# Optimization experiments

Measured on AMD Instinct MI355X. Metric: run time of the kernel, lower is better.

The kernel has to match this reference:

```python
import jax, jax.numpy as jnp
import numpy as np

D = 128; H = 8; DH = D // H
N = 50000; B = 8; MAXN = N // B
E = 400000
NG_G = 4; NG_L = 4; NG = NG_G + NG_L
DFF = 2 * D


def _ln(x, eps=1e-5):
    m = x.mean(-1, keepdims=True)
    v = ((x - m) ** 2).mean(-1, keepdims=True)
    return (x - m) * jax.lax.rsqrt(v + eps)


def _mha(q, k, v, in_w, in_b, out_w, out_b):
    # torch nn.MultiheadAttention (batch_first, eval) with packed in_proj
    Bq, Lq, d = q.shape; Lk = k.shape[1]
    wq, wk, wv = jnp.split(in_w, 3, axis=0)
    bq, bk, bv = jnp.split(in_b, 3)
    Q = (q @ wq.T + bq).reshape(Bq, Lq, H, DH).transpose(0, 2, 1, 3)
    K = (k @ wk.T + bk).reshape(Bq, Lk, H, DH).transpose(0, 2, 1, 3)
    V = (v @ wv.T + bv).reshape(Bq, Lk, H, DH).transpose(0, 2, 1, 3)
    A = jax.nn.softmax(jnp.einsum('bhqd,bhkd->bhqk', Q, K) / np.float32(np.sqrt(DH)), axis=-1)
    O = jnp.einsum('bhqk,bhkd->bhqd', A, V).transpose(0, 2, 1, 3).reshape(Bq, Lq, d)
    return O @ out_w.T + out_b, A.mean(axis=1)  # averaged attn weights over heads


def _tconv(x, src, dst, Wq, bq, Wk, bk, Wv, bv, Wskip, bskip, Wbeta):
    # PyG TransformerConv(d, d//H, heads=H, beta=True): edge-wise gather-attend-scatter
    n = x.shape[0]
    q = (x @ Wq.T + bq)[dst].reshape(-1, H, DH)   # [E,H,DH] query at target node
    k = (x @ Wk.T + bk)[src].reshape(-1, H, DH)
    v = (x @ Wv.T + bv)[src].reshape(-1, H, DH)
    logits = (q * k).sum(-1) / np.float32(np.sqrt(DH))  # [E,H]
    m = jax.ops.segment_max(logits, dst, num_segments=n)
    m = jnp.where(jnp.isfinite(m), m, 0.0)
    a = jnp.exp(logits - m[dst])
    s = jax.ops.segment_sum(a, dst, num_segments=n)
    alpha = a / (s[dst] + 1e-16)                  # per-target-node softmax (PyG softmax)
    out = jax.ops.segment_sum(v * alpha[..., None], dst, num_segments=n).reshape(n, D)
    xr = x @ Wskip.T + bskip                      # root weight
    beta = jax.nn.sigmoid(jnp.concatenate([out, xr, out - xr], axis=-1) @ Wbeta.T)
    return beta * xr + (1.0 - beta) * out


def setup_inputs() -> dict:
    key = jax.random.key(0)
    ks = jax.random.split(key, 16)
    w = lambda i, shape, s=0.05: jax.random.normal(ks[i], shape, jnp.float32) * s
    return dict(
        x=w(0, (N, D), 1.0),
        edge_index=jax.random.randint(ks[1], (2, E), 0, N),
        global_h=w(2, (B, NG, D), 1.0),
        batch=jnp.repeat(jnp.arange(B, dtype=jnp.int32), MAXN),  # sorted, even split
        n_global_tokens_global=NG_G,
        n_global_tokens_local=NG_L,
        Wq=w(3, (D, D)), bq=jnp.zeros((D,), jnp.float32),
        Wk=w(4, (D, D)), bk=jnp.zeros((D,), jnp.float32),
        Wv=w(5, (D, D)), bv=jnp.zeros((D,), jnp.float32),
        Wskip=w(6, (D, D)), bskip=jnp.zeros((D,), jnp.float32),
        Wbeta=w(7, (1, 3 * D)),
        ng_in_w=w(8, (3 * D, D)), ng_in_b=jnp.zeros((3 * D,), jnp.float32),
        ng_out_w=w(9, (D, D)), ng_out_b=jnp.zeros((D,), jnp.float32),
        gn_in_w=w(10, (3 * D, D)), gn_in_b=jnp.zeros((3 * D,), jnp.float32),
        gn_out_w=w(11, (D, D)), gn_out_b=jnp.zeros((D,), jnp.float32),
        W1=w(12, (DFF, D)), b1=jnp.zeros((DFF,), jnp.float32),
        W2=w(13, (D, DFF)), b2=jnp.zeros((D,), jnp.float32),
    )


def reference(x, edge_index, global_h, batch, n_global_tokens_global, n_global_tokens_local,
              Wq, bq, Wk, bk, Wv, bv, Wskip, bskip, Wbeta,
              ng_in_w, ng_in_b, ng_out_w, ng_out_b,
              gn_in_w, gn_in_b, gn_out_w, gn_out_b,
              W1, b1, W2, b2):
    src, dst = edge_index[0], edge_index[1]
    h_local = _tconv(x, src, dst, Wq, bq, Wk, bk, Wv, bv, Wskip, bskip, Wbeta)
    x = _ln(x + h_local)
    Bg = global_h.shape[0]
    # to_dense_batch: batch is sorted with equal-size graphs -> mask all True, pure reshape
    dense_x = x.reshape(Bg, -1, D)
    global_out, attn_w = _mha(global_h, dense_x, dense_x, ng_in_w, ng_in_b, ng_out_w, ng_out_b)
    global_h = _ln(global_h + global_out)
    nodes_out, _ = _mha(dense_x, global_h, global_h, gn_in_w, gn_in_b, gn_out_w, gn_out_b)
    dense_x = _ln(dense_x + nodes_out)
    x = dense_x.reshape(-1, D)  # un-scatter (even split -> reshape)
    ff = jax.nn.relu(x @ W1.T + b1) @ W2.T + b2
    x = _ln(x + ff)
    # attention regularization, vectorized over the per-graph python loop
    ls = n_global_tokens_global
    le = ls + n_global_tokens_local
    P = attn_w[:, ls:le, :]                      # [B, K, max_n], all nodes valid
    Pn = P / (P.sum(-1, keepdims=True) + 1e-8)
    G = jnp.einsum('bkn,bmn->bkm', Pn, Pn)       # [B, K, K]
    Kt = le - ls
    off = (G.sum(axis=(1, 2)) - jnp.einsum('bkk->b', G)) / (Kt * Kt - Kt)
    reg = off.mean()
    return x, global_h, reg
```

## Files before the change

kernel.cpp:

```cpp
#include <hip/hip_runtime.h>
#include <math.h>

#define D 128
#define H 8
#define NGT 8
#define LSTOK 4
#define NCH 4

typedef short bf16x8 __attribute__((ext_vector_type(8)));
typedef float f32x4  __attribute__((ext_vector_type(4)));

__device__ __forceinline__ short f2bf(float f) {
  union { float f; unsigned u; } v; v.f = f;
  unsigned r = v.u + 0x7FFFu + ((v.u >> 16) & 1u);
  return (short)(r >> 16);
}
__device__ __forceinline__ float bf2f(short s) {
  union { unsigned u; float f; } v;
  v.u = ((unsigned)(unsigned short)s) << 16;
  return v.f;
}
__device__ __forceinline__ float4 bf4(bf16x8 v, int lo) {
  return make_float4(bf2f(v[lo]), bf2f(v[lo + 1]), bf2f(v[lo + 2]), bf2f(v[lo + 3]));
}
__device__ __forceinline__ unsigned pk2(float a, float b) {
  return ((unsigned)(unsigned short)f2bf(b) << 16) | (unsigned short)f2bf(a);
}

__device__ __forceinline__ float dot4(float4 a, float4 b) {
  return a.x*b.x + a.y*b.y + a.z*b.z + a.w*b.w;
}
__device__ __forceinline__ float4 scale_madd(float4 a, float sc, float4 v, float p) {
  return make_float4(fmaf(p, v.x, a.x*sc), fmaf(p, v.y, a.y*sc),
                     fmaf(p, v.z, a.z*sc), fmaf(p, v.w, a.w*sc));
}
__device__ __forceinline__ float4 comb4(float4 a, float e1, float4 c, float e2) {
  return make_float4(a.x*e1 + c.x*e2, a.y*e1 + c.y*e2, a.z*e1 + c.z*e2, a.w*e1 + c.w*e2);
}
__device__ __forceinline__ float4 shfl_xor4(float4 v, int off) {
  return make_float4(__shfl_xor(v.x, off), __shfl_xor(v.y, off),
                     __shfl_xor(v.z, off), __shfl_xor(v.w, off));
}

struct CvtArgs {
  const float* s[10];
  short*       d[10];
  int          n[10];
};

__global__ void cvt_weights(CvtArgs a) {
  int which = blockIdx.y;
  const float* s = a.s[which];
  short* d = a.d[which];
  int n = a.n[which];
  int i = (blockIdx.x * 256 + threadIdx.x) * 4;
  if (i + 3 < n) {
    float4 v = *(const float4*)(s + i);
    d[i]     = f2bf(v.x);
    d[i + 1] = f2bf(v.y);
    d[i + 2] = f2bf(v.z);
    d[i + 3] = f2bf(v.w);
  }
}

__global__ void cvt_x(const float* __restrict__ s, short* __restrict__ d, int n) {
  int i = (blockIdx.x * 256 + threadIdx.x) * 8;
  if (i + 7 < n) {
    float4 a = *(const float4*)(s + i);
    float4 b = *(const float4*)(s + i + 4);
    bf16x8 v;
    v[0] = f2bf(a.x); v[1] = f2bf(a.y); v[2] = f2bf(a.z); v[3] = f2bf(a.w);
    v[4] = f2bf(b.x); v[5] = f2bf(b.y); v[6] = f2bf(b.z); v[7] = f2bf(b.w);
    *(bf16x8*)(d + i) = v;
  }
}

__global__ void concat_bias4(const float* __restrict__ b0, const float* __restrict__ b1,
                             const float* __restrict__ b2, const float* __restrict__ b3,
                             float* __restrict__ out) {
  int t = threadIdx.x;
  out[t] = b0[t]; out[128 + t] = b1[t]; out[256 + t] = b2[t]; out[384 + t] = b3[t];
}

#define EPST 72
template<int K>
__global__ void __launch_bounds__(256) gemm_direct(const short* __restrict__ A,
    const short* __restrict__ Wb, const float* __restrict__ bias,
    short* __restrict__ out16, int C16, int s16,
    float* __restrict__ out32, int s32,
    int Nrows, int Ccols, int relu)
{
  __shared__ short eplds[4][64 * EPST];
  const int t = threadIdx.x;
  const int wid = t >> 6, lane = t & 63;
  const int rowBase = blockIdx.x * 128 + (wid >> 1) * 64;
  const int colBase = blockIdx.y * 128 + (wid & 1) * 64;
  const int lrow = lane & 15;
  const int lk = (lane >> 4) * 8;

  f32x4 acc[4][4];
  f32x4 z4 = {0.f, 0.f, 0.f, 0.f};
#pragma unroll
  for (int m = 0; m < 4; m++)
#pragma unroll
    for (int n = 0; n < 4; n++) acc[m][n] = z4;

  const short* ap[4];
#pragma unroll
  for (int m = 0; m < 4; ++m) {
    int ar = rowBase + m * 16 + lrow;
    if (ar >= Nrows) ar = Nrows - 1;
    ap[m] = A + (size_t)ar * K + lk;
  }
  const short* wp[4];
#pragma unroll
  for (int n = 0; n < 4; ++n)
    wp[n] = Wb + (size_t)(colBase + n * 16 + lrow) * K + lk;

#pragma unroll
  for (int kb = 0; kb < K; kb += 32) {
    bf16x8 af[4], bfr[4];
#pragma unroll
    for (int m = 0; m < 4; ++m) af[m] = *(const bf16x8*)(ap[m] + kb);
#pragma unroll
    for (int n = 0; n < 4; ++n) bfr[n] = *(const bf16x8*)(wp[n] + kb);
#pragma unroll
    for (int m = 0; m < 4; ++m)
#pragma unroll
      for (int n = 0; n < 4; ++n)
        acc[m][n] = __builtin_amdgcn_mfma_f32_16x16x32_bf16(af[m], bfr[n], acc[m][n], 0, 0, 0);
  }

  const int ccol = lane & 15;
  const int rquad = (lane >> 4) * 4;
  if (colBase < C16) {
    short* lds = eplds[wid];
#pragma unroll
    for (int n = 0; n < 4; ++n) {
      float bb = bias[colBase + n * 16 + ccol];
      int col = n * 16 + ccol;
#pragma unroll
      for (int m = 0; m < 4; ++m) {
        int r0 = m * 16 + rquad;
#pragma unroll
        for (int r = 0; r < 4; ++r) {
          float v = acc[m][n][r] + bb;
          if (relu) v = fmaxf(v, 0.f);
          lds[(r0 + r) * EPST + col] = f2bf(v);
        }
      }
    }
    const int jr = lane >> 3, jc = lane & 7;
#pragma unroll
    for (int i = 0; i < 8; ++i) {
      int row = i * 8 + jr;
      int gr = rowBase + row;
      if (gr < Nrows) {
        bf16x8 v = *(const bf16x8*)(lds + row * EPST + jc * 8);
        *(bf16x8*)(out16 + (size_t)gr * s16 + colBase + jc * 8) = v;
      }
    }
  } else {
#pragma unroll
    for (int n = 0; n < 4; ++n) {
      int col = colBase + n * 16 + ccol;
      float bb = bias[col];
#pragma unroll
      for (int m = 0; m < 4; ++m) {
        int row0 = rowBase + m * 16 + rquad;
#pragma unroll
        for (int r = 0; r < 4; ++r) {
          int gr = row0 + r;
          if (gr < Nrows) {
            float v = acc[m][n][r] + bb;
            if (relu) v = fmaxf(v, 0.f);
            out32[(size_t)gr * s32 + (col - C16)] = v;
          }
        }
      }
    }
  }
}

#define FFST 264
__global__ void __launch_bounds__(256) gemm_ff(const short* __restrict__ A,
    const short* __restrict__ W1b, const float* __restrict__ b1,
    const short* __restrict__ W2b, const float* __restrict__ b2,
    float* __restrict__ out, int Nrows)
{
  __shared__ short flds[128 * FFST];
  const int t = threadIdx.x;
  const int wid = t >> 6, lane = t & 63;
  const int rowL = (wid >> 1) * 64;
  const int rowBase = blockIdx.x * 128 + rowL;
  const int lrow = lane & 15;
  const int lk = (lane >> 4) * 8;
  const int ccol = lane & 15;
  const int rquad = (lane >> 4) * 4;
  f32x4 z4 = {0.f, 0.f, 0.f, 0.f};

  const short* ap[4];
#pragma unroll
  for (int m = 0; m < 4; ++m) {
    int ar = rowBase + m * 16 + lrow;
    if (ar >= Nrows) ar = Nrows - 1;
    ap[m] = A + (size_t)ar * 128 + lk;
  }

  for (int cb = 0; cb < 2; ++cb) {
    int colBase = cb * 128 + (wid & 1) * 64;
    f32x4 acc[4][4];
#pragma unroll
    for (int m = 0; m < 4; m++)
#pragma unroll
      for (int n = 0; n < 4; n++) acc[m][n] = z4;
    const short* wp[4];
#pragma unroll
    for (int n = 0; n < 4; ++n)
      wp[n] = W1b + (size_t)(colBase + n * 16 + lrow) * 128 + lk;
#pragma unroll
    for (int kb = 0; kb < 128; kb += 32) {
      bf16x8 af[4], bfr[4];
#pragma unroll
      for (int m = 0; m < 4; ++m) af[m] = *(const bf16x8*)(ap[m] + kb);
#pragma unroll
      for (int n = 0; n < 4; ++n) bfr[n] = *(const bf16x8*)(wp[n] + kb);
#pragma unroll
      for (int m = 0; m < 4; ++m)
#pragma unroll
        for (int n = 0; n < 4; ++n)
          acc[m][n] = __builtin_amdgcn_mfma_f32_16x16x32_bf16(af[m], bfr[n], acc[m][n], 0, 0, 0);
    }
#pragma unroll
    for (int n = 0; n < 4; ++n) {
      int col = colBase + n * 16 + ccol;
      float bb = b1[col];
#pragma unroll
      for (int m = 0; m < 4; ++m) {
        int r0 = rowL + m * 16 + rquad;
#pragma unroll
        for (int r = 0; r < 4; ++r) {
          float v = fmaxf(acc[m][n][r] + bb, 0.f);
          flds[(r0 + r) * FFST + col] = f2bf(v);
        }
      }
    }
  }
  __syncthreads();

  {
    int colBase = (wid & 1) * 64;
    f32x4 acc[4][4];
#pragma unroll
    for (int m = 0; m < 4; m++)
#pragma unroll
      for (int n = 0; n < 4; n++) acc[m][n] = z4;
    const short* wp[4];
#pragma unroll
    for (int n = 0; n < 4; ++n)
      wp[n] = W2b + (size_t)(colBase + n * 16 + lrow) * 256 + lk;
#pragma unroll
    for (int kb = 0; kb < 256; kb += 32) {
      bf16x8 af[4], bfr[4];
#pragma unroll
      for (int m = 0; m < 4; ++m)
        af[m] = *(const bf16x8*)(flds + (rowL + m * 16 + lrow) * FFST + kb + lk);
#pragma unroll
      for (int n = 0; n < 4; ++n) bfr[n] = *(const bf16x8*)(wp[n] + kb);
#pragma unroll
      for (int m = 0; m < 4; ++m)
#pragma unroll
        for (int n = 0; n < 4; ++n)
          acc[m][n] = __builtin_amdgcn_mfma_f32_16x16x32_bf16(af[m], bfr[n], acc[m][n], 0, 0, 0);
    }
#pragma unroll
    for (int n = 0; n < 4; ++n) {
      int col = colBase + n * 16 + ccol;
      float bb = b2[col];
#pragma unroll
      for (int m = 0; m < 4; ++m) {
        int row0 = rowBase + m * 16 + rquad;
#pragma unroll
        for (int r = 0; r < 4; ++r) {
          int gr = row0 + r;
          if (gr < Nrows) out[(size_t)gr * 128 + col] = acc[m][n][r] + bb;
        }
      }
    }
  }
}

#define QST 136
__global__ void __launch_bounds__(256) gemm_node(const short* __restrict__ A,
    const short* __restrict__ GnQb, const float* __restrict__ gnbq,
    const float* __restrict__ Kg, const float* __restrict__ Vg,
    const short* __restrict__ GnOb, const float* __restrict__ gnbo,
    float* __restrict__ out, int Nrows, int MAXN)
{
  __shared__ short qlds[128 * QST];
  __shared__ float kg[2][NGT * 128];
  __shared__ float vg[2][NGT * 128];
  const int t = threadIdx.x;
  const int wid = t >> 6, lane = t & 63;
  const int rowL = (wid >> 1) * 64;
  const int n0 = blockIdx.x * 128;
  const int rowBase = n0 + rowL;
  const int colBase = (wid & 1) * 64;
  const int lrow = lane & 15;
  const int lk = (lane >> 4) * 8;
  const int ccol = lane & 15;
  const int rquad = (lane >> 4) * 4;
  f32x4 z4 = {0.f, 0.f, 0.f, 0.f};

  int b0 = n0 / MAXN;
  int nlast = n0 + 127; if (nlast >= Nrows) nlast = Nrows - 1;
  int bLast = nlast / MAXN;
  int nb = (bLast != b0) ? 2 : 1;
  for (int bi = 0; bi < nb; ++bi) {
    size_t gb = (size_t)((b0 + bi) * NGT) * 128;
    int i = t * 4;
    *(float4*)&kg[bi][i] = *(const float4*)(Kg + gb + i);
    *(float4*)&vg[bi][i] = *(const float4*)(Vg + gb + i);
  }

  {
    f32x4 acc[4][4];
#pragma unroll
    for (int m = 0; m < 4; m++)
#pragma unroll
      for (int n = 0; n < 4; n++) acc[m][n] = z4;
    const short* ap[4];
#pragma unroll
    for (int m = 0; m < 4; ++m) {
      int ar = rowBase + m * 16 + lrow;
      if (ar >= Nrows) ar = Nrows - 1;
      ap[m] = A + (size_t)ar * 128 + lk;
    }
    const short* wp[4];
#pragma unroll
    for (int n = 0; n < 4; ++n)
      wp[n] = GnQb + (size_t)(colBase + n * 16 + lrow) * 128 + lk;
#pragma unroll
    for (int kb = 0; kb < 128; kb += 32) {
      bf16x8 af[4], bfr[4];
#pragma unroll
      for (int m = 0; m < 4; ++m) af[m] = *(const bf16x8*)(ap[m] + kb);
#pragma unroll
      for (int n = 0; n < 4; ++n) bfr[n] = *(const bf16x8*)(wp[n] + kb);
#pragma unroll
      for (int m = 0; m < 4; ++m)
#pragma unroll
        for (int n = 0; n < 4; ++n)
          acc[m][n] = __builtin_amdgcn_mfma_f32_16x16x32_bf16(af[m], bfr[n], acc[m][n], 0, 0, 0);
    }
#pragma unroll
    for (int n = 0; n < 4; ++n) {
      int col = colBase + n * 16 + ccol;
      float bb = gnbq[col];
#pragma unroll
      for (int m = 0; m < 4; ++m) {
        int r0 = rowL + m * 16 + rquad;
#pragma unroll
        for (int r = 0; r < 4; ++r)
          qlds[(r0 + r) * QST + col] = f2bf(acc[m][n][r] + bb);
      }
    }
  }
  __syncthreads();

#pragma unroll
  for (int u = 0; u < 4; ++u) {
    int unit = t + u * 256;
    int row = unit >> 3, h = unit & 7;
    int grow = n0 + row;
    if (grow < Nrows) {
      int bi = (grow / MAXN) - b0;
      short* qp = qlds + row * QST + h * 16;
      bf16x8 qa = *(const bf16x8*)(qp);
      bf16x8 qb = *(const bf16x8*)(qp + 8);
      float4 q0 = bf4(qa, 0), q1 = bf4(qa, 4), q2 = bf4(qb, 0), q3 = bf4(qb, 4);
      float l[NGT];
      float mx = -3.0e38f;
#pragma unroll
      for (int tk = 0; tk < NGT; tk++) {
        const float4* k4 = (const float4*)(&kg[bi][tk * 128 + h * 16]);
        float d = dot4(q0, k4[0]) + dot4(q1, k4[1]) + dot4(q2, k4[2]) + dot4(q3, k4[3]);
        l[tk] = d * 0.25f;
        mx = fmaxf(mx, l[tk]);
      }
      float s = 0.f;
#pragma unroll
      for (int tk = 0; tk < NGT; tk++) { l[tk] = expf(l[tk] - mx); s += l[tk]; }
      float inv = 1.f / s;
      float4 a0 = make_float4(0, 0, 0, 0), a1 = a0, a2 = a0, a3 = a0;
#pragma unroll
      for (int tk = 0; tk < NGT; tk++) {
        float p = l[tk] * inv;
        const float4* v4 = (const float4*)(&vg[bi][tk * 128 + h * 16]);
        a0 = scale_madd(a0, 1.f, v4[0], p);
        a1 = scale_madd(a1, 1.f, v4[1], p);
        a2 = scale_madd(a2, 1.f, v4[2], p);
        a3 = scale_madd(a3, 1.f, v4[3], p);
      }
      unsigned* o = (unsigned*)qp;
      o[0] = pk2(a0.x, a0.y); o[1] = pk2(a0.z, a0.w);
      o[2] = pk2(a1.x, a1.y); o[3] = pk2(a1.z, a1.w);
      o[4] = pk2(a2.x, a2.y); o[5] = pk2(a2.z, a2.w);
      o[6] = pk2(a3.x, a3.y); o[7] = pk2(a3.z, a3.w);
    }
  }
  __syncthreads();

  {
    f32x4 acc[4][4];
#pragma unroll
    for (int m = 0; m < 4; m++)
#pragma unroll
      for (int n = 0; n < 4; n++) acc[m][n] = z4;
    const short* wp[4];
#pragma unroll
    for (int n = 0; n < 4; ++n)
      wp[n] = GnOb + (size_t)(colBase + n * 16 + lrow) * 128 + lk;
#pragma unroll
    for (int kb = 0; kb < 128; kb += 32) {
      bf16x8 af[4], bfr[4];
#pragma unroll
      for (int m = 0; m < 4; ++m)
        af[m] = *(const bf16x8*)(qlds + (rowL + m * 16 + lrow) * QST + kb + lk);
#pragma unroll
      for (int n = 0; n < 4; ++n) bfr[n] = *(const bf16x8*)(wp[n] + kb);
#pragma unroll
      for (int m = 0; m < 4; ++m)
#pragma unroll
        for (int n = 0; n < 4; ++n)
          acc[m][n] = __builtin_amdgcn_mfma_f32_16x16x32_bf16(af[m], bfr[n], acc[m][n], 0, 0, 0);
    }
#pragma unroll
    for (int n = 0; n < 4; ++n) {
      int col = colBase + n * 16 + ccol;
      float bb = gnbo[col];
#pragma unroll
      for (int m = 0; m < 4; ++m) {
        int row0 = rowBase + m * 16 + rquad;
#pragma unroll
        for (int r = 0; r < 4; ++r) {
          int gr = row0 + r;
          if (gr < Nrows) out[(size_t)gr * 128 + col] = acc[m][n][r] + bb;
        }
      }
    }
  }
}

__global__ void gemm_small(const float* __restrict__ A, const float* __restrict__ W,
                           const float* __restrict__ bias, float* __restrict__ out, int M)
{
  int r = blockIdx.x;
  int c = threadIdx.x;
  __shared__ float as[128];
  as[c] = A[(size_t)r * 128 + c];
  __syncthreads();
  float acc = bias[c];
  const float* wr = W + (size_t)c * 128;
#pragma unroll 4
  for (int k = 0; k < 128; k++) acc += as[k] * wr[k];
  out[(size_t)r * 128 + c] = acc;
}

__global__ void count_deg(const int* __restrict__ dst, int* __restrict__ deg, int E) {
  int e = blockIdx.x * 256 + threadIdx.x;
  if (e < E) atomicAdd(&deg[dst[e]], 1);
}

__global__ void scan_pass1(const int* __restrict__ deg, int* __restrict__ bsum, int N) {
  int t = threadIdx.x, lane = t & 63, wid = t >> 6;
  int idx = blockIdx.x * 1024 + t * 4;
  int4 v = {0, 0, 0, 0};
  if (idx + 3 < N) v = *(const int4*)(deg + idx);
  else {
    if (idx < N) v.x = deg[idx];
    if (idx + 1 < N) v.y = deg[idx + 1];
    if (idx + 2 < N) v.z = deg[idx + 2];
    if (idx + 3 < N) v.w = deg[idx + 3];
  }
  int s = v.x + v.y + v.z + v.w;
#pragma unroll
  for (int off = 32; off >= 1; off >>= 1) s += __shfl_xor(s, off);
  __shared__ int ws[4];
  if (lane == 0) ws[wid] = s;
  __syncthreads();
  if (t == 0) bsum[blockIdx.x] = ws[0] + ws[1] + ws[2] + ws[3];
}

__global__ void scan_pass2(int* __restrict__ bsum, int SB) {
  __shared__ int sh[1024];
  int t = threadIdx.x;
  sh[t] = (t < SB) ? bsum[t] : 0;
  __syncthreads();
  for (int off = 1; off < 1024; off <<= 1) {
    int v = (t >= off) ? sh[t - off] : 0;
    __syncthreads();
    sh[t] += v;
    __syncthreads();
  }
  if (t < SB) bsum[t] = (t == 0) ? 0 : sh[t - 1];
}

__global__ void scan_pass3(const int* __restrict__ deg, const int* __restrict__ bsum,
                           int* __restrict__ row_start, int* __restrict__ cursor,
                           int N, int E)
{
  int t = threadIdx.x, lane = t & 63, wid = t >> 6;
  int idx = blockIdx.x * 1024 + t * 4;
  int4 v = {0, 0, 0, 0};
  if (idx + 3 < N) v = *(const int4*)(deg + idx);
  else {
    if (idx < N) v.x = deg[idx];
    if (idx + 1 < N) v.y = deg[idx + 1];
    if (idx + 2 < N) v.z = deg[idx + 2];
    if (idx + 3 < N) v.w = deg[idx + 3];
  }
  int ts = v.x + v.y + v.z + v.w;
  int x = ts;
#pragma unroll
  for (int off = 1; off < 64; off <<= 1) {
    int y = __shfl_up(x, off);
    if (lane >= off) x += y;
  }
  __shared__ int ws[4];
  if (lane == 63) ws[wid] = x;
  __syncthreads();
  int woff = 0;
  for (int i = 0; i < wid; i++) woff += ws[i];
  int p = bsum[blockIdx.x] + woff + (x - ts);
  if (idx < N)     { row_start[idx] = p; cursor[idx] = p; }     p += v.x;
  if (idx + 1 < N) { row_start[idx + 1] = p; cursor[idx + 1] = p; } p += v.y;
  if (idx + 2 < N) { row_start[idx + 2] = p; cursor[idx + 2] = p; } p += v.z;
  if (idx + 3 < N) { row_start[idx + 3] = p; cursor[idx + 3] = p; }
  if (blockIdx.x == 0 && t == 0) row_start[N] = E;
}

__global__ void fill_edges(const int* __restrict__ dst, const int* __restrict__ src,
                           int* __restrict__ cursor, int* __restrict__ edge_src, int E) {
  int e = blockIdx.x * 256 + threadIdx.x;
  if (e < E) {
    int p = atomicAdd(&cursor[dst[e]], 1);
    edge_src[p] = src[e];
  }
}

__global__ void tconv_attn(const short* __restrict__ qkvb,
                           const int* __restrict__ row_start,
                           const int* __restrict__ edge_src,
                           float* __restrict__ out, int N)
{
  int gid = blockIdx.x * 256 + threadIdx.x;
  if (gid >= N * H) return;
  int n = gid >> 3, h = gid & 7;
  const short* qp = qkvb + (size_t)n * 512 + h * 16;
  bf16x8 qa = *(const bf16x8*)(qp);
  bf16x8 qb = *(const bf16x8*)(qp + 8);
  float4 q0 = bf4(qa, 0), q1 = bf4(qa, 4), q2 = bf4(qb, 0), q3 = bf4(qb, 4);
  int e0 = row_start[n], e1 = row_start[n + 1];

  float mA = -3.0e38f, sA = 0.f;
  float4 A0 = make_float4(0, 0, 0, 0), A1 = A0, A2 = A0, A3 = A0;
  float mB = -3.0e38f, sB = 0.f;
  float4 B0 = A0, B1 = A0, B2 = A0, B3 = A0;

  int ei = e0;
  for (; ei + 1 < e1; ei += 2) {
    int sn0 = edge_src[ei], sn1 = edge_src[ei + 1];
    const short* kp0 = qkvb + (size_t)sn0 * 512 + 128 + h * 16;
    const short* kp1 = qkvb + (size_t)sn1 * 512 + 128 + h * 16;
    bf16x8 k00 = *(const bf16x8*)(kp0);
    bf16x8 k01 = *(const bf16x8*)(kp0 + 8);
    bf16x8 k10 = *(const bf16x8*)(kp1);
    bf16x8 k11 = *(const bf16x8*)(kp1 + 8);
    float d0 = (dot4(q0, bf4(k00, 0)) + dot4(q1, bf4(k00, 4))
              + dot4(q2, bf4(k01, 0)) + dot4(q3, bf4(k01, 4))) * 0.25f;
    float d1 = (dot4(q0, bf4(k10, 0)) + dot4(q1, bf4(k10, 4))
              + dot4(q2, bf4(k11, 0)) + dot4(q3, bf4(k11, 4))) * 0.25f;
    bf16x8 v00 = *(const bf16x8*)(kp0 + 128);
    bf16x8 v01 = *(const bf16x8*)(kp0 + 136);
    bf16x8 v10 = *(const bf16x8*)(kp1 + 128);
    bf16x8 v11 = *(const bf16x8*)(kp1 + 136);
    float mn0 = fmaxf(mA, d0);
    float sc0 = expf(mA - mn0), p0 = expf(d0 - mn0);
    A0 = scale_madd(A0, sc0, bf4(v00, 0), p0);
    A1 = scale_madd(A1, sc0, bf4(v00, 4), p0);
    A2 = scale_madd(A2, sc0, bf4(v01, 0), p0);
    A3 = scale_madd(A3, sc0, bf4(v01, 4), p0);
    sA = sA * sc0 + p0; mA = mn0;
    float mn1 = fmaxf(mB, d1);
    float sc1 = expf(mB - mn1), p1 = expf(d1 - mn1);
    B0 = scale_madd(B0, sc1, bf4(v10, 0), p1);
    B1 = scale_madd(B1, sc1, bf4(v10, 4), p1);
    B2 = scale_madd(B2, sc1, bf4(v11, 0), p1);
    B3 = scale_madd(B3, sc1, bf4(v11, 4), p1);
    sB = sB * sc1 + p1; mB = mn1;
  }
  if (ei < e1) {
    int sn0 = edge_src[ei];
    const short* kp0 = qkvb + (size_t)sn0 * 512 + 128 + h * 16;
    bf16x8 k00 = *(const bf16x8*)(kp0);
    bf16x8 k01 = *(const bf16x8*)(kp0 + 8);
    float d0 = (dot4(q0, bf4(k00, 0)) + dot4(q1, bf4(k00, 4))
              + dot4(q2, bf4(k01, 0)) + dot4(q3, bf4(k01, 4))) * 0.25f;
    bf16x8 v00 = *(const bf16x8*)(kp0 + 128);
    bf16x8 v01 = *(const bf16x8*)(kp0 + 136);
    float mn0 = fmaxf(mA, d0);
    float sc0 = expf(mA - mn0), p0 = expf(d0 - mn0);
    A0 = scale_madd(A0, sc0, bf4(v00, 0), p0);
    A1 = scale_madd(A1, sc0, bf4(v00, 4), p0);
    A2 = scale_madd(A2, sc0, bf4(v01, 0), p0);
    A3 = scale_madd(A3, sc0, bf4(v01, 4), p0);
    sA = sA * sc0 + p0; mA = mn0;
  }
  float mn = fmaxf(mA, mB);
  float eA = expf(mA - mn), eB = expf(mB - mn);
  float s = sA * eA + sB * eB;
  float4 a0 = comb4(A0, eA, B0, eB);
  float4 a1 = comb4(A1, eA, B1, eB);
  float4 a2 = comb4(A2, eA, B2, eB);
  float4 a3 = comb4(A3, eA, B3, eB);
  float inv = 1.f / (s + 1e-16f);
  float4* o4 = (float4*)(out + (size_t)n * 128 + h * 16);
  o4[0] = make_float4(a0.x * inv, a0.y * inv, a0.z * inv, a0.w * inv);
  o4[1] = make_float4(a1.x * inv, a1.y * inv, a1.z * inv, a1.w * inv);
  o4[2] = make_float4(a2.x * inv, a2.y * inv, a2.z * inv, a2.w * inv);
  o4[3] = make_float4(a3.x * inv, a3.y * inv, a3.z * inv, a3.w * inv);
}

__global__ void gate_ln(const float* __restrict__ x, const float* __restrict__ att,
                        const short* __restrict__ qkvb, const float* __restrict__ Wb,
                        float* __restrict__ x1, short* __restrict__ x1b, int N)
{
  int wid = threadIdx.x >> 6, lane = threadIdx.x & 63;
  int n = blockIdx.x * 4 + wid;
  if (n >= N) return;
  size_t base = (size_t)n * 128 + lane * 2;
  float2 o = *(const float2*)(att + base);
  unsigned ru = *(const unsigned*)(qkvb + (size_t)n * 512 + 384 + lane * 2);
  float2 r = make_float2(bf2f((short)(ru & 0xFFFF)), bf2f((short)(ru >> 16)));
  float2 xv = *(const float2*)(x + base);
  float2 w0 = *(const float2*)(Wb + lane * 2);
  float2 w1 = *(const float2*)(Wb + 128 + lane * 2);
  float2 w2 = *(const float2*)(Wb + 256 + lane * 2);
  float ts = o.x * w0.x + o.y * w0.y + r.x * w1.x + r.y * w1.y
           + (o.x - r.x) * w2.x + (o.y - r.y) * w2.y;
#pragma unroll
  for (int mm = 32; mm >= 1; mm >>= 1) ts += __shfl_xor(ts, mm);
  float beta = 1.f / (1.f + expf(-ts));
  float2 y;
  y.x = xv.x + beta * r.x + (1.f - beta) * o.x;
  y.y = xv.y + beta * r.y + (1.f - beta) * o.y;
  float sm = y.x + y.y;
#pragma unroll
  for (int mm = 32; mm >= 1; mm >>= 1) sm += __shfl_xor(sm, mm);
  float mean = sm * (1.f / 128.f);
  float dx = y.x - mean, dy = y.y - mean;
  float vs = dx * dx + dy * dy;
#pragma unroll
  for (int mm = 32; mm >= 1; mm >>= 1) vs += __shfl_xor(vs, mm);
  float rstd = rsqrtf(vs * (1.f / 128.f) + 1e-5f);
  float ox = dx * rstd, oy = dy * rstd;
  *(float2*)(x1 + base) = make_float2(ox, oy);
  *(unsigned*)(x1b + base) = pk2(ox, oy);
}

__global__ void ln_add(const float* __restrict__ a, const float* __restrict__ b,
                       float* __restrict__ out, short* __restrict__ out16, int R)
{
  int wid = threadIdx.x >> 6, lane = threadIdx.x & 63;
  int r = blockIdx.x * 4 + wid;
  if (r >= R) return;
  size_t base = (size_t)r * 128 + lane * 2;
  float2 av = *(const float2*)(a + base);
  float2 bv = *(const float2*)(b + base);
  float2 y = make_float2(av.x + bv.x, av.y + bv.y);
  float sm = y.x + y.y;
#pragma unroll
  for (int mm = 32; mm >= 1; mm >>= 1) sm += __shfl_xor(sm, mm);
  float mean = sm * (1.f / 128.f);
  float dx = y.x - mean, dy = y.y - mean;
  float vs = dx * dx + dy * dy;
#pragma unroll
  for (int mm = 32; mm >= 1; mm >>= 1) vs += __shfl_xor(vs, mm);
  float rstd = rsqrtf(vs * (1.f / 128.f) + 1e-5f);
  float ox = dx * rstd, oy = dy * rstd;
  *(float2*)(out + base) = make_float2(ox, oy);
  if (out16) *(unsigned*)(out16 + base) = pk2(ox, oy);
}

__global__ void glob_part(const float* __restrict__ Qg, const short* __restrict__ kv,
                          float* __restrict__ Plog,
                          float* __restrict__ pm, float* __restrict__ ps,
                          float* __restrict__ pacc, int MAXN)
{
  int blk = blockIdx.x;
  int ch = blockIdx.y;
  int h = blk & 7, g = (blk >> 3) & 7, b = blk >> 6;
  int lane = threadIdx.x;
  const float4* q4 = (const float4*)(Qg + (size_t)(b * NGT + g) * 128 + h * 16);
  float4 q0 = q4[0], q1 = q4[1], q2 = q4[2], q3 = q4[3];
  int chunk = (MAXN + NCH - 1) / NCH;
  int n0 = ch * chunk;
  int n1 = n0 + chunk; if (n1 > MAXN) n1 = MAXN;
  float* plrow = (g >= LSTOK) ? Plog + (((size_t)(b * 4 + g - LSTOK)) * H + h) * MAXN : nullptr;
  float m = -3.0e38f, s = 0.f;
  float4 a0 = make_float4(0, 0, 0, 0), a1 = a0, a2 = a0, a3 = a0;
  for (int n = n0 + lane; n < n1; n += 64) {
    const short* kp = kv + ((size_t)(b * MAXN + n)) * 256 + h * 16;
    bf16x8 k0 = *(const bf16x8*)(kp);
    bf16x8 k1 = *(const bf16x8*)(kp + 8);
    float d = dot4(q0, bf4(k0, 0)) + dot4(q1, bf4(k0, 4))
            + dot4(q2, bf4(k1, 0)) + dot4(q3, bf4(k1, 4));
    d *= 0.25f;
    if (plrow) plrow[n] = d;
    float mn = fmaxf(m, d);
    float sc = expf(m - mn);
    float p = expf(d - mn);
    bf16x8 v0 = *(const bf16x8*)(kp + 128);
    bf16x8 v1 = *(const bf16x8*)(kp + 136);
    a0 = scale_madd(a0, sc, bf4(v0, 0), p);
    a1 = scale_madd(a1, sc, bf4(v0, 4), p);
    a2 = scale_madd(a2, sc, bf4(v1, 0), p);
    a3 = scale_madd(a3, sc, bf4(v1, 4), p);
    s = s * sc + p;
    m = mn;
  }
#pragma unroll
  for (int off = 32; off >= 1; off >>= 1) {
    float m2 = __shfl_xor(m, off);
    float s2 = __shfl_xor(s, off);
    float4 c0 = shfl_xor4(a0, off), c1 = shfl_xor4(a1, off);
    float4 c2 = shfl_xor4(a2, off), c3 = shfl_xor4(a3, off);
    float mn = fmaxf(m, m2);
    float e1 = expf(m - mn), e2 = expf(m2 - mn);
    s = s * e1 + s2 * e2;
    a0 = comb4(a0, e1, c0, e2);
    a1 = comb4(a1, e1, c1, e2);
    a2 = comb4(a2, e1, c2, e2);
    a3 = comb4(a3, e1, c3, e2);
    m = mn;
  }
  if (lane == 0) {
    int pi = blk * NCH + ch;
    pm[pi] = m; ps[pi] = s;
    float4* pa = (float4*)(pacc + (size_t)pi * 16);
    pa[0] = a0; pa[1] = a1; pa[2] = a2; pa[3] = a3;
  }
}

__global__ void glob_merge(const float* __restrict__ pm, const float* __restrict__ ps,
                           const float* __restrict__ pacc, float* __restrict__ Og,
                           float* __restrict__ m_gl, float* __restrict__ is_gl)
{
  int blk = blockIdx.x;
  int lane = threadIdx.x;
  float m = -3.0e38f;
#pragma unroll
  for (int c = 0; c < NCH; ++c) m = fmaxf(m, pm[blk * NCH + c]);
  float s = 0.f;
#pragma unroll
  for (int c = 0; c < NCH; ++c) s += ps[blk * NCH + c] * expf(pm[blk * NCH + c] - m);
  if (lane < 16) {
    float a = 0.f;
#pragma unroll
    for (int c = 0; c < NCH; ++c)
      a += pacc[(size_t)(blk * NCH + c) * 16 + lane] * expf(pm[blk * NCH + c] - m);
    int h = blk & 7, g = (blk >> 3) & 7, b = blk >> 6;
    Og[(size_t)(b * NGT + g) * 128 + h * 16 + lane] = a / s;
  }
  if (lane == 0) { m_gl[blk] = m; is_gl[blk] = 1.f / s; }
}

__global__ void pker2(const float* __restrict__ Plog,
                      const float* __restrict__ m_gl, const float* __restrict__ is_gl,
                      float* __restrict__ P, int MAXN)
{
  int b = blockIdx.y;
  __shared__ float ms[32], iss[32];
  if (threadIdx.x < 32) {
    int g = threadIdx.x >> 3, h = threadIdx.x & 7;
    ms[threadIdx.x]  = m_gl[(b * NGT + LSTOK + g) * H + h];
    iss[threadIdx.x] = is_gl[(b * NGT + LSTOK + g) * H + h];
  }
  __syncthreads();
  int n = blockIdx.x * 256 + threadIdx.x;
  if (n >= MAXN) return;
#pragma unroll
  for (int g = 0; g < 4; g++) {
    float acc = 0.f;
#pragma unroll
    for (int h = 0; h < H; h++) {
      float l = Plog[(((size_t)(b * 4 + g)) * H + h) * MAXN + n];
      acc += expf(l - ms[g * 8 + h]) * iss[g * 8 + h];
    }
    P[(size_t)(b * 4 + g) * MAXN + n] = acc * 0.125f;
  }
}

__global__ void regk(const float* __restrict__ P, float* __restrict__ offb, int MAXN)
{
  int b = blockIdx.x;
  int t = threadIdx.x;
  float v[10];
#pragma unroll
  for (int i = 0; i < 10; i++) v[i] = 0.f;
  for (int n = t; n < MAXN; n += 256) {
    float p0 = P[(size_t)(b * 4 + 0) * MAXN + n];
    float p1 = P[(size_t)(b * 4 + 1) * MAXN + n];
    float p2 = P[(size_t)(b * 4 + 2) * MAXN + n];
    float p3 = P[(size_t)(b * 4 + 3) * MAXN + n];
    v[0] += p0; v[1] += p1; v[2] += p2; v[3] += p3;
    v[4] += p0 * p1; v[5] += p0 * p2; v[6] += p0 * p3;
    v[7] += p1 * p2; v[8] += p1 * p3; v[9] += p2 * p3;
  }
#pragma unroll
  for (int i = 0; i < 10; i++) {
    float x = v[i];
#pragma unroll
    for (int mm = 32; mm >= 1; mm >>= 1) x += __shfl_xor(x, mm);
    v[i] = x;
  }
  __shared__ float red[4][10];
  int wid = t >> 6, lane = t & 63;
  if (lane == 0)
    for (int i = 0; i < 10; i++) red[wid][i] = v[i];
  __syncthreads();
  if (t == 0) {
    float r[10];
    for (int i = 0; i < 10; i++) r[i] = red[0][i] + red[1][i] + red[2][i] + red[3][i];
    float r0 = r[0] + 1e-8f, r1 = r[1] + 1e-8f, r2 = r[2] + 1e-8f, r3 = r[3] + 1e-8f;
    float off = 2.f * (r[4] / (r0 * r1) + r[5] / (r0 * r2) + r[6] / (r0 * r3)
                     + r[7] / (r1 * r2) + r[8] / (r1 * r3) + r[9] / (r2 * r3));
    offb[b] = off * (1.f / 12.f);
  }
}

__global__ void regfin(const float* __restrict__ offb, float* __restrict__ out) {
  if (threadIdx.x == 0 && blockIdx.x == 0) {
    float s = 0.f;
    for (int i = 0; i < 8; i++) s += offb[i];
    *out = s * (1.f / 8.f);
  }
}

extern "C" void kernel_launch(void* const* d_in, const int* in_sizes, int n_in,
                              void* d_out, int out_size, void* d_ws, size_t ws_size,
                              hipStream_t stream)
{
  const float* x     = (const float*)d_in[0];
  const int*   ei    = (const int*)d_in[1];
  const float* gh    = (const float*)d_in[2];
  const float* Wq    = (const float*)d_in[6];
  const float* bqv   = (const float*)d_in[7];
  const float* Wk    = (const float*)d_in[8];
  const float* bkv   = (const float*)d_in[9];
  const float* Wv    = (const float*)d_in[10];
  const float* bvv   = (const float*)d_in[11];
  const float* Wsk   = (const float*)d_in[12];
  const float* bsk   = (const float*)d_in[13];
  const float* Wbeta = (const float*)d_in[14];
  const float* ngw   = (const float*)d_in[15];
  const float* ngb   = (const float*)d_in[16];
  const float* ngow  = (const float*)d_in[17];
  const float* ngob  = (const float*)d_in[18];
  const float* gnw   = (const float*)d_in[19];
  const float* gnb   = (const float*)d_in[20];
  const float* gnow  = (const float*)d_in[21];
  const float* gnob  = (const float*)d_in[22];
  const float* W1    = (const float*)d_in[23];
  const float* b1v   = (const float*)d_in[24];
  const float* W2    = (const float*)d_in[25];
  const float* b2v   = (const float*)d_in[26];

  const int N    = in_sizes[0] / D;
  const int E    = in_sizes[1] / 2;
  const int Bb   = 8;
  const int MAXN = N / Bb;

  const int* srcI = ei;
  const int* dstI = ei + E;

  size_t NF = (size_t)N;
  size_t ND = NF * D;
  float* fw = (float*)d_ws;
  short* qkvb = (short*)fw;
  short* kv16 = qkvb;
  float* ff2o = fw + NF * 256;
  float* x1   = fw + NF * 384;
  short* x1b  = (short*)(fw + NF * 512);
  float* misc = fw + NF * 576;
  float* Qg    = misc;
  float* Og    = Qg + 8192;
  float* gout  = Og + 8192;
  float* Kg    = gout + 8192;
  float* Vg    = Kg + 8192;
  float* m_gl  = Vg + 8192;
  float* is_gl = m_gl + 512;
  float* Pbuf  = is_gl + 512;
  float* offb  = Pbuf + (size_t)Bb * 4 * MAXN;
  float* bias512 = offb + 16;
  float* Plog  = bias512 + 512;
  float* pm    = Plog + (size_t)4 * H * Bb * MAXN;
  float* ps    = pm + 512 * NCH;
  float* pacc  = ps + 512 * NCH;
  int* deg       = (int*)(pacc + 512 * NCH * 16);
  int* row_start = deg + N;
  int* cursor    = row_start + N + 1;
  int* bsum      = cursor + N;
  int* edge_src  = bsum + 1024;
  short* wbase = (short*)((((uintptr_t)(edge_src + E)) + 15) & ~(uintptr_t)15);
  short* cWq  = wbase;
  short* cWk  = cWq  + 16384;
  short* cWv  = cWk  + 16384;
  short* cWsk = cWv  + 16384;
  short* cNgK = cWsk + 16384;
  short* cNgV = cNgK + 16384;
  short* cGnQ = cNgV + 16384;
  short* cGnO = cGnQ + 16384;
  short* cW1  = cGnO + 16384;
  short* cW2  = cW1  + 32768;
  short* xb   = cW2  + 32768;

  float* outx   = (float*)d_out;
  float* outgh  = outx + ND;
  float* outreg = outgh + (size_t)Bb * NGT * D;
  float* wa     = outx;

  const int GXM = (N + 127) / 128;
  const int SB  = (N + 1023) / 1024;
  dim3 blk256(256);

  CvtArgs ca;
  ca.s[0] = Wq;   ca.d[0] = cWq;  ca.n[0] = 16384;
  ca.s[1] = Wk;   ca.d[1] = cWk;  ca.n[1] = 16384;
  ca.s[2] = Wv;   ca.d[2] = cWv;  ca.n[2] = 16384;
  ca.s[3] = Wsk;  ca.d[3] = cWsk; ca.n[3] = 16384;
  ca.s[4] = ngw + 128 * 128; ca.d[4] = cNgK; ca.n[4] = 16384;
  ca.s[5] = ngw + 256 * 128; ca.d[5] = cNgV; ca.n[5] = 16384;
  ca.s[6] = gnw;  ca.d[6] = cGnQ; ca.n[6] = 16384;
  ca.s[7] = gnow; ca.d[7] = cGnO; ca.n[7] = 16384;
  ca.s[8] = W1;   ca.d[8] = cW1;  ca.n[8] = 32768;
  ca.s[9] = W2;   ca.d[9] = cW2;  ca.n[9] = 32768;
  cvt_weights<<<dim3(32, 10), blk256, 0, stream>>>(ca);
  concat_bias4<<<dim3(1), dim3(128), 0, stream>>>(bqv, bkv, bvv, bsk, bias512);
  cvt_x<<<dim3((N * 128 / 8 + 255) / 256), blk256, 0, stream>>>(x, xb, N * 128);

  hipMemsetAsync(deg, 0, (size_t)N * sizeof(int), stream);
  count_deg<<<dim3((E + 255) / 256), blk256, 0, stream>>>(dstI, deg, E);
  scan_pass1<<<dim3(SB), blk256, 0, stream>>>(deg, bsum, N);
  scan_pass2<<<dim3(1), dim3(1024), 0, stream>>>(bsum, SB);
  scan_pass3<<<dim3(SB), blk256, 0, stream>>>(deg, bsum, row_start, cursor, N, E);
  fill_edges<<<dim3((E + 255) / 256), blk256, 0, stream>>>(dstI, srcI, cursor, edge_src, E);

  gemm_direct<128><<<dim3(GXM, 4), blk256, 0, stream>>>(xb, cWq, bias512,
                                                        qkvb, 512, 512, nullptr, 0,
                                                        N, 512, 0);

  tconv_attn<<<dim3((N * H + 255) / 256), blk256, 0, stream>>>(qkvb, row_start, edge_src, wa, N);
  gate_ln<<<dim3((N + 3) / 4), blk256, 0, stream>>>(x, wa, qkvb, Wbeta, x1, x1b, N);

  gemm_direct<128><<<dim3(GXM, 2), blk256, 0, stream>>>(x1b, cNgK, ngb + 128,
                                                        kv16, 256, 256, nullptr, 0,
                                                        N, 256, 0);
  gemm_small<<<dim3(64), dim3(128), 0, stream>>>(gh, ngw, ngb, Qg, 64);
  glob_part<<<dim3(512, NCH), dim3(64), 0, stream>>>(Qg, kv16, Plog, pm, ps, pacc, MAXN);
  glob_merge<<<dim3(512), dim3(64), 0, stream>>>(pm, ps, pacc, Og, m_gl, is_gl);
  pker2<<<dim3((MAXN + 255) / 256, 8), blk256, 0, stream>>>(Plog, m_gl, is_gl, Pbuf, MAXN);
  regk<<<dim3(8), blk256, 0, stream>>>(Pbuf, offb, MAXN);
  regfin<<<dim3(1), dim3(64), 0, stream>>>(offb, outreg);

  gemm_small<<<dim3(64), dim3(128), 0, stream>>>(Og, ngow, ngob, gout, 64);
  ln_add<<<dim3(16), blk256, 0, stream>>>(gh, gout, outgh, nullptr, 64);

  gemm_small<<<dim3(64), dim3(128), 0, stream>>>(outgh, gnw + 128 * 128, gnb + 128, Kg, 64);
  gemm_small<<<dim3(64), dim3(128), 0, stream>>>(outgh, gnw + 256 * 128, gnb + 256, Vg, 64);
  gemm_node<<<dim3(GXM), blk256, 0, stream>>>(x1b, cGnQ, gnb, Kg, Vg, cGnO, gnob,
                                              wa, N, MAXN);
  ln_add<<<dim3((N + 3) / 4), blk256, 0, stream>>>(x1, wa, x1, x1b, N);

  gemm_ff<<<dim3(GXM), blk256, 0, stream>>>(x1b, cW1, b1v, cW2, b2v, ff2o, N);
  ln_add<<<dim3((N + 3) / 4), blk256, 0, stream>>>(x1, ff2o, outx, nullptr, N);
}
```

Before: 361.3 us.

## Split fused node-to-global attention kernel into GEMM, attention, GEMM launches

Replaces the fused gemm_node kernel (Q projection, per-node attention over 8 global tokens, and output projection all held in LDS) with three launches. A generic gemm_direct writes Q in bf16, a new node_attn kernel computes the attention per (node, head), and a second gemm_direct applies the output projection. This un-fusion probably aims to improve occupancy, since the fused kernel used large LDS and serialised its phases. In exchange it adds global round-trips of two N×128 bf16 buffers and extra launch overhead.

```diff
diff --git a/kernel.cpp b/kernel.cpp
--- a/kernel.cpp
+++ b/kernel.cpp
@@ -277,168 +277,6 @@
     for (int n = 0; n < 4; ++n) {
       int col = colBase + n * 16 + ccol;
       float bb = b2[col];
-#pragma unroll
-      for (int m = 0; m < 4; ++m) {
-        int row0 = rowBase + m * 16 + rquad;
-#pragma unroll
-        for (int r = 0; r < 4; ++r) {
-          int gr = row0 + r;
-          if (gr < Nrows) out[(size_t)gr * 128 + col] = acc[m][n][r] + bb;
-        }
-      }
-    }
-  }
-}
-
-#define QST 136
-__global__ void __launch_bounds__(256) gemm_node(const short* __restrict__ A,
-    const short* __restrict__ GnQb, const float* __restrict__ gnbq,
-    const float* __restrict__ Kg, const float* __restrict__ Vg,
-    const short* __restrict__ GnOb, const float* __restrict__ gnbo,
-    float* __restrict__ out, int Nrows, int MAXN)
-{
-  __shared__ short qlds[128 * QST];
-  __shared__ float kg[2][NGT * 128];
-  __shared__ float vg[2][NGT * 128];
-  const int t = threadIdx.x;
-  const int wid = t >> 6, lane = t & 63;
-  const int rowL = (wid >> 1) * 64;
-  const int n0 = blockIdx.x * 128;
-  const int rowBase = n0 + rowL;
-  const int colBase = (wid & 1) * 64;
-  const int lrow = lane & 15;
-  const int lk = (lane >> 4) * 8;
-  const int ccol = lane & 15;
-  const int rquad = (lane >> 4) * 4;
-  f32x4 z4 = {0.f, 0.f, 0.f, 0.f};
-
-  int b0 = n0 / MAXN;
-  int nlast = n0 + 127; if (nlast >= Nrows) nlast = Nrows - 1;
-  int bLast = nlast / MAXN;
-  int nb = (bLast != b0) ? 2 : 1;
-  for (int bi = 0; bi < nb; ++bi) {
-    size_t gb = (size_t)((b0 + bi) * NGT) * 128;
-    int i = t * 4;
-    *(float4*)&kg[bi][i] = *(const float4*)(Kg + gb + i);
-    *(float4*)&vg[bi][i] = *(const float4*)(Vg + gb + i);
-  }
-
-  {
-    f32x4 acc[4][4];
-#pragma unroll
-    for (int m = 0; m < 4; m++)
-#pragma unroll
-      for (int n = 0; n < 4; n++) acc[m][n] = z4;
-    const short* ap[4];
-#pragma unroll
-    for (int m = 0; m < 4; ++m) {
-      int ar = rowBase + m * 16 + lrow;
-      if (ar >= Nrows) ar = Nrows - 1;
-      ap[m] = A + (size_t)ar * 128 + lk;
-    }
-    const short* wp[4];
-#pragma unroll
-    for (int n = 0; n < 4; ++n)
-      wp[n] = GnQb + (size_t)(colBase + n * 16 + lrow) * 128 + lk;
-#pragma unroll
-    for (int kb = 0; kb < 128; kb += 32) {
-      bf16x8 af[4], bfr[4];
-#pragma unroll
-      for (int m = 0; m < 4; ++m) af[m] = *(const bf16x8*)(ap[m] + kb);
-#pragma unroll
-      for (int n = 0; n < 4; ++n) bfr[n] = *(const bf16x8*)(wp[n] + kb);
-#pragma unroll
-      for (int m = 0; m < 4; ++m)
-#pragma unroll
-        for (int n = 0; n < 4; ++n)
-          acc[m][n] = __builtin_amdgcn_mfma_f32_16x16x32_bf16(af[m], bfr[n], acc[m][n], 0, 0, 0);
-    }
-#pragma unroll
-    for (int n = 0; n < 4; ++n) {
-      int col = colBase + n * 16 + ccol;
-      float bb = gnbq[col];
-#pragma unroll
-      for (int m = 0; m < 4; ++m) {
-        int r0 = rowL + m * 16 + rquad;
-#pragma unroll
-        for (int r = 0; r < 4; ++r)
-          qlds[(r0 + r) * QST + col] = f2bf(acc[m][n][r] + bb);
-      }
-    }
-  }
-  __syncthreads();
-
-#pragma unroll
-  for (int u = 0; u < 4; ++u) {
-    int unit = t + u * 256;
-    int row = unit >> 3, h = unit & 7;
-    int grow = n0 + row;
-    if (grow < Nrows) {
-      int bi = (grow / MAXN) - b0;
-      short* qp = qlds + row * QST + h * 16;
-      bf16x8 qa = *(const bf16x8*)(qp);
-      bf16x8 qb = *(const bf16x8*)(qp + 8);
-      float4 q0 = bf4(qa, 0), q1 = bf4(qa, 4), q2 = bf4(qb, 0), q3 = bf4(qb, 4);
-      float l[NGT];
-      float mx = -3.0e38f;
-#pragma unroll
-      for (int tk = 0; tk < NGT; tk++) {
-        const float4* k4 = (const float4*)(&kg[bi][tk * 128 + h * 16]);
-        float d = dot4(q0, k4[0]) + dot4(q1, k4[1]) + dot4(q2, k4[2]) + dot4(q3, k4[3]);
-        l[tk] = d * 0.25f;
-        mx = fmaxf(mx, l[tk]);
-      }
-      float s = 0.f;
-#pragma unroll
-      for (int tk = 0; tk < NGT; tk++) { l[tk] = expf(l[tk] - mx); s += l[tk]; }
-      float inv = 1.f / s;
-      float4 a0 = make_float4(0, 0, 0, 0), a1 = a0, a2 = a0, a3 = a0;
-#pragma unroll
-      for (int tk = 0; tk < NGT; tk++) {
-        float p = l[tk] * inv;
-        const float4* v4 = (const float4*)(&vg[bi][tk * 128 + h * 16]);
-        a0 = scale_madd(a0, 1.f, v4[0], p);
-        a1 = scale_madd(a1, 1.f, v4[1], p);
-        a2 = scale_madd(a2, 1.f, v4[2], p);
-        a3 = scale_madd(a3, 1.f, v4[3], p);
-      }
-      unsigned* o = (unsigned*)qp;
-      o[0] = pk2(a0.x, a0.y); o[1] = pk2(a0.z, a0.w);
-      o[2] = pk2(a1.x, a1.y); o[3] = pk2(a1.z, a1.w);
-      o[4] = pk2(a2.x, a2.y); o[5] = pk2(a2.z, a2.w);
-      o[6] = pk2(a3.x, a3.y); o[7] = pk2(a3.z, a3.w);
-    }
-  }
-  __syncthreads();
-
-  {
-    f32x4 acc[4][4];
-#pragma unroll
-    for (int m = 0; m < 4; m++)
-#pragma unroll
-      for (int n = 0; n < 4; n++) acc[m][n] = z4;
-    const short* wp[4];
-#pragma unroll
-    for (int n = 0; n < 4; ++n)
-      wp[n] = GnOb + (size_t)(colBase + n * 16 + lrow) * 128 + lk;
-#pragma unroll
-    for (int kb = 0; kb < 128; kb += 32) {
-      bf16x8 af[4], bfr[4];
-#pragma unroll
-      for (int m = 0; m < 4; ++m)
-        af[m] = *(const bf16x8*)(qlds + (rowL + m * 16 + lrow) * QST + kb + lk);
-#pragma unroll
-      for (int n = 0; n < 4; ++n) bfr[n] = *(const bf16x8*)(wp[n] + kb);
-#pragma unroll
-      for (int m = 0; m < 4; ++m)
-#pragma unroll
-        for (int n = 0; n < 4; ++n)
-          acc[m][n] = __builtin_amdgcn_mfma_f32_16x16x32_bf16(af[m], bfr[n], acc[m][n], 0, 0, 0);
-    }
-#pragma unroll
-    for (int n = 0; n < 4; ++n) {
-      int col = colBase + n * 16 + ccol;
-      float bb = gnbo[col];
 #pragma unroll
       for (int m = 0; m < 4; ++m) {
         int row0 = rowBase + m * 16 + rquad;
@@ -848,6 +686,61 @@
   }
 }
 
+__global__ void node_attn(const short* __restrict__ Qn, const float* __restrict__ Kg,
+                          const float* __restrict__ Vg, short* __restrict__ On,
+                          int N, int MAXN)
+{
+  __shared__ float kg[2][NGT * 128];
+  __shared__ float vg[2][NGT * 128];
+  int n0 = blockIdx.x * 32;
+  int b0 = n0 / MAXN;
+  int nlast = n0 + 31; if (nlast >= N) nlast = N - 1;
+  int bLast = nlast / MAXN;
+  int nb = (bLast != b0) ? 2 : 1;
+  for (int bi = 0; bi < nb; ++bi) {
+    size_t gb = (size_t)((b0 + bi) * NGT) * 128;
+    int i = threadIdx.x * 4;
+    *(float4*)&kg[bi][i] = *(const float4*)(Kg + gb + i);
+    *(float4*)&vg[bi][i] = *(const float4*)(Vg + gb + i);
+  }
+  __syncthreads();
+  int n = n0 + (threadIdx.x >> 3), h = threadIdx.x & 7;
+  if (n >= N) return;
+  int bi = (n / MAXN) - b0;
+  const short* qp = Qn + (size_t)n * 128 + h * 16;
+  bf16x8 qa = *(const bf16x8*)(qp);
+  bf16x8 qb = *(const bf16x8*)(qp + 8);
+  float4 q0 = bf4(qa, 0), q1 = bf4(qa, 4), q2 = bf4(qb, 0), q3 = bf4(qb, 4);
+  float l[NGT];
+  float mx = -3.0e38f;
+#pragma unroll
+  for (int tk = 0; tk < NGT; tk++) {
+    const float4* k4 = (const float4*)(&kg[bi][tk * 128 + h * 16]);
+    float d = dot4(q0, k4[0]) + dot4(q1, k4[1]) + dot4(q2, k4[2]) + dot4(q3, k4[3]);
+    l[tk] = d * 0.25f;
+    mx = fmaxf(mx, l[tk]);
+  }
+  float s = 0.f;
+#pragma unroll
+  for (int tk = 0; tk < NGT; tk++) { l[tk] = expf(l[tk] - mx); s += l[tk]; }
+  float inv = 1.f / s;
+  float4 a0 = make_float4(0, 0, 0, 0), a1 = a0, a2 = a0, a3 = a0;
+#pragma unroll
+  for (int tk = 0; tk < NGT; tk++) {
+    float p = l[tk] * inv;
+    const float4* v4 = (const float4*)(&vg[bi][tk * 128 + h * 16]);
+    a0 = scale_madd(a0, 1.f, v4[0], p);
+    a1 = scale_madd(a1, 1.f, v4[1], p);
+    a2 = scale_madd(a2, 1.f, v4[2], p);
+    a3 = scale_madd(a3, 1.f, v4[3], p);
+  }
+  unsigned* o = (unsigned*)(On + (size_t)n * 128 + h * 16);
+  o[0] = pk2(a0.x, a0.y); o[1] = pk2(a0.z, a0.w);
+  o[2] = pk2(a1.x, a1.y); o[3] = pk2(a1.z, a1.w);
+  o[4] = pk2(a2.x, a2.y); o[5] = pk2(a2.z, a2.w);
+  o[6] = pk2(a3.x, a3.y); o[7] = pk2(a3.z, a3.w);
+}
+
 extern "C" void kernel_launch(void* const* d_in, const int* in_sizes, int n_in,
                               void* d_out, int out_size, void* d_ws, size_t ws_size,
                               hipStream_t stream)
@@ -890,6 +783,8 @@
   float* fw = (float*)d_ws;
   short* qkvb = (short*)fw;
   short* kv16 = qkvb;
+  short* Qnb  = qkvb + NF * 256;
+  short* Onb  = qkvb + NF * 384;
   float* ff2o = fw + NF * 256;
   float* x1   = fw + NF * 384;
   short* x1b  = (short*)(fw + NF * 512);
@@ -979,8 +874,13 @@
 
   gemm_small<<<dim3(64), dim3(128), 0, stream>>>(outgh, gnw + 128 * 128, gnb + 128, Kg, 64);
   gemm_small<<<dim3(64), dim3(128), 0, stream>>>(outgh, gnw + 256 * 128, gnb + 256, Vg, 64);
-  gemm_node<<<dim3(GXM), blk256, 0, stream>>>(x1b, cGnQ, gnb, Kg, Vg, cGnO, gnob,
-                                              wa, N, MAXN);
+  gemm_direct<128><<<dim3(GXM, 1), blk256, 0, stream>>>(x1b, cGnQ, gnb,
+                                                        Qnb, 128, 128, nullptr, 0,
+                                                        N, 128, 0);
+  node_attn<<<dim3((N + 31) / 32), blk256, 0, stream>>>(Qnb, Kg, Vg, Onb, N, MAXN);
+  gemm_direct<128><<<dim3(GXM, 1), blk256, 0, stream>>>(Onb, cGnO, gnob,
+                                                        nullptr, 0, 0, wa, 128,
+                                                        N, 128, 0);
   ln_add<<<dim3((N + 3) / 4), blk256, 0, stream>>>(x1, wa, x1, x1b, N);
 
   gemm_ff<<<dim3(GXM), blk256, 0, stream>>>(x1b, cW1, b1v, cW2, b2v, ff2o, N);
```

Result: no change. 367.4 us (+1.7%).
